# Kernel tuning notes

Measured on AMD Instinct MI355X. Metric: run time of the kernel, lower is better.

Reference implementation:

```python
import math
import jax, jax.numpy as jnp
import numpy as np

DIM = 4096
N_HEADS = 32
N_KV_HEADS = 8
HEAD_DIM = DIM // N_HEADS  # 128
N_REP = N_HEADS // N_KV_HEADS  # 4
BSZ = 2
SEQLEN = 2048
ROPE_THETA = 500000.0


def setup_inputs() -> dict:
    key = jax.random.key(0)
    ks = jax.random.split(key, 6)
    s = 0.02
    x = jax.random.normal(ks[0], (BSZ, SEQLEN, DIM), dtype=jnp.float32)
    wq = jax.random.normal(ks[1], (DIM, N_HEADS * HEAD_DIM), dtype=jnp.float32) * s
    wk = jax.random.normal(ks[2], (DIM, N_KV_HEADS * HEAD_DIM), dtype=jnp.float32) * s
    wv = jax.random.normal(ks[3], (DIM, N_KV_HEADS * HEAD_DIM), dtype=jnp.float32) * s
    wo = jax.random.normal(ks[4], (N_HEADS * HEAD_DIM, DIM), dtype=jnp.float32) * s
    # RoPE frequencies (real cos/sin form of complex freqs_cis)
    inv_freq = 1.0 / (ROPE_THETA ** (jnp.arange(0, HEAD_DIM, 2, dtype=jnp.float32) / HEAD_DIM))
    t = jnp.arange(SEQLEN, dtype=jnp.float32)
    angles = jnp.outer(t, inv_freq)  # [S, HEAD_DIM/2]
    freqs_cos = jnp.cos(angles)
    freqs_sin = jnp.sin(angles)
    # additive causal mask [S, S]: 0 on/below diag, -1e9 above
    mask = jnp.where(jnp.tril(jnp.ones((SEQLEN, SEQLEN), dtype=bool)), 0.0, -1e9).astype(jnp.float32)
    return {"x": x, "wq": wq, "wk": wk, "wv": wv, "wo": wo,
            "freqs_cos": freqs_cos, "freqs_sin": freqs_sin, "mask": mask,
            "start_pos": 0}


def _apply_rope(t, cos, sin):
    # t: [B, S, H, HD]; cos/sin: [S, HD/2] -> broadcast [1, S, 1, HD/2]
    b, s, h, hd = t.shape
    tr = t.reshape(b, s, h, hd // 2, 2)
    te, to = tr[..., 0], tr[..., 1]
    c = cos[None, :, None, :]
    sn = sin[None, :, None, :]
    oe = te * c - to * sn
    oo = te * sn + to * c
    return jnp.stack([oe, oo], axis=-1).reshape(b, s, h, hd)


def reference(x, wq, wk, wv, wo, freqs_cos, freqs_sin, mask, start_pos):
    bsz, seqlen, _ = x.shape
    xq = (x @ wq).reshape(bsz, seqlen, N_HEADS, HEAD_DIM)
    xk = (x @ wk).reshape(bsz, seqlen, N_KV_HEADS, HEAD_DIM)
    xv = (x @ wv).reshape(bsz, seqlen, N_KV_HEADS, HEAD_DIM)
    xq = _apply_rope(xq, freqs_cos, freqs_sin)
    xk = _apply_rope(xk, freqs_cos, freqs_sin)
    # prefill: cache[:start_pos+seqlen] == xk/xv (start_pos=0); GQA repeat
    keys = jnp.repeat(xk, N_REP, axis=2)    # [B, S, N_HEADS, HD]
    values = jnp.repeat(xv, N_REP, axis=2)
    q = xq.transpose(0, 2, 1, 3)            # [B, H, S, HD]
    k = keys.transpose(0, 2, 1, 3)
    v = values.transpose(0, 2, 1, 3)
    scores = jnp.einsum('bhqd,bhkd->bhqk', q, k) / math.sqrt(HEAD_DIM)
    scores = scores + mask[None, None, :, :]
    probs = jax.nn.softmax(scores.astype(jnp.float32), axis=-1).astype(q.dtype)
    ctx = jnp.einsum('bhqk,bhkd->bhqd', probs, v)
    out = ctx.transpose(0, 2, 1, 3).reshape(bsz, seqlen, N_HEADS * HEAD_DIM)
    return out @ wo
```

## Files before the change

kernel.cpp:

```cpp
#include <hip/hip_runtime.h>
#include <hip/hip_bf16.h>
#include <math.h>
#include <stdint.h>

#define DIM 4096
#define N_HEADS 32
#define N_KV_HEADS 8
#define HEAD_DIM 128
#define BSZ 2
#define SEQLEN 2048
#define BS (BSZ * SEQLEN)
#define KV_DIM (N_KV_HEADS * HEAD_DIM)

typedef unsigned short u16;
typedef __attribute__((ext_vector_type(8))) short bf16x8;
typedef __attribute__((ext_vector_type(4))) float f32x4;
typedef __attribute__((ext_vector_type(8))) unsigned short u16x8;
typedef __attribute__((ext_vector_type(4))) unsigned short u16x4;

__device__ __forceinline__ u16 f2bf(float f) {
    __hip_bfloat16 h = __float2bfloat16(f);
    return *reinterpret_cast<u16*>(&h);
}
__device__ __forceinline__ float bf2f(u16 u) {
    __hip_bfloat16 h;
    *reinterpret_cast<u16*>(&h) = u;
    return __bfloat162float(h);
}

#define GLOAD_LDS16(gptr, lptr)                                                      \
    __builtin_amdgcn_global_load_lds(                                                \
        reinterpret_cast<const __attribute__((address_space(1))) uint32_t*>(         \
            reinterpret_cast<uintptr_t>(gptr)),                                      \
        reinterpret_cast<__attribute__((address_space(3))) uint32_t*>(               \
            reinterpret_cast<uintptr_t>(lptr)),                                      \
        16, 0, 0)

__global__ void cvt_f32_bf16(const float* __restrict__ in, u16* __restrict__ out, int n4) {
    int i = blockIdx.x * blockDim.x + threadIdx.x;
    if (i >= n4) return;
    float4 v = reinterpret_cast<const float4*>(in)[i];
    u16x4 o;
    o.x = f2bf(v.x); o.y = f2bf(v.y); o.z = f2bf(v.z); o.w = f2bf(v.w);
    reinterpret_cast<u16x4*>(out)[i] = o;
}

__global__ __launch_bounds__(256) void transpose_f32_bf16(const float* __restrict__ in,
                                                          u16* __restrict__ out,
                                                          int K, int N) {
    __shared__ float tile[32][33];
    const int tx = threadIdx.x, ty = threadIdx.y;
    const int n0 = blockIdx.x * 32, k0 = blockIdx.y * 32;
#pragma unroll
    for (int i = 0; i < 4; ++i)
        tile[ty + 8 * i][tx] = in[(size_t)(k0 + ty + 8 * i) * N + n0 + tx];
    __syncthreads();
#pragma unroll
    for (int i = 0; i < 4; ++i)
        out[(size_t)(n0 + ty + 8 * i) * K + k0 + tx] = f2bf(tile[tx][ty + 8 * i]);
}

__global__ __launch_bounds__(256) void transpose_v_bf16(const u16* __restrict__ xv,
                                                        u16* __restrict__ xvT) {
    __shared__ u16 tile[32][33];
    const int tx = threadIdx.x, ty = threadIdx.y;
    const int k0 = blockIdx.x * 32, d0 = blockIdx.y * 32;
    const int bh = blockIdx.z;
    const int b = bh >> 3, hkv = bh & 7;
#pragma unroll
    for (int i = 0; i < 4; ++i)
        tile[ty + 8 * i][tx] =
            xv[((size_t)(b * SEQLEN) + k0 + ty + 8 * i) * KV_DIM + hkv * HEAD_DIM + d0 + tx];
    __syncthreads();
#pragma unroll
    for (int i = 0; i < 4; ++i)
        xvT[((size_t)bh * HEAD_DIM + d0 + ty + 8 * i) * SEQLEN + k0 + tx] = tile[tx][ty + 8 * i];
}

template <bool OUT_BF16>
__global__ __launch_bounds__(256) void gemm_mfma_bt(const u16* __restrict__ A,
                                                    const u16* __restrict__ BT,
                                                    void* __restrict__ Cv,
                                                    int M, int N, int K) {
    __shared__ __align__(16) u16 Al[128 * 64];
    __shared__ __align__(16) u16 Bl[128 * 64];

    const int tid  = threadIdx.x;
    const int wave = tid >> 6;
    const int lane = tid & 63;
    const int quad = lane >> 4;
    const int lm   = lane & 15;
    const size_t bm = (size_t)blockIdx.y * 128;
    const size_t bn = (size_t)blockIdx.x * 128;
    const int wm = (wave & 1) * 64;
    const int wn = (wave >> 1) * 64;

    const int slot = lane & 7;
    const int lrow = lane >> 3;
    const int csw  = slot ^ (lrow & 7);

    f32x4 acc[4][4] = {};

    for (int k0 = 0; k0 < K; k0 += 64) {
        __syncthreads();
#pragma unroll
        for (int i = 0; i < 4; ++i) {
            const int mloc = wave * 32 + i * 8 + lrow;
            const u16* gA = A  + (bm + mloc) * (size_t)K + k0 + csw * 8;
            const u16* gB = BT + (bn + mloc) * (size_t)K + k0 + csw * 8;
            u16* lA = &Al[(mloc * 8 + slot) * 8];
            u16* lB = &Bl[(mloc * 8 + slot) * 8];
            GLOAD_LDS16(gA, lA);
            GLOAD_LDS16(gB, lB);
        }
        __syncthreads();

#pragma unroll
        for (int ks8 = 0; ks8 < 8; ks8 += 4) {
            bf16x8 af[4], bfr[4];
            const int cc = ks8 + quad;
#pragma unroll
            for (int i = 0; i < 4; ++i) {
                const int m = wm + 16 * i + lm;
                af[i]  = *(const bf16x8*)&Al[(m * 8 + (cc ^ (m & 7))) * 8];
                const int n = wn + 16 * i + lm;
                bfr[i] = *(const bf16x8*)&Bl[(n * 8 + (cc ^ (n & 7))) * 8];
            }
#pragma unroll
            for (int i = 0; i < 4; ++i)
#pragma unroll
                for (int j = 0; j < 4; ++j)
                    acc[i][j] = __builtin_amdgcn_mfma_f32_16x16x32_bf16(af[i], bfr[j], acc[i][j], 0, 0, 0);
        }
    }

#pragma unroll
    for (int i = 0; i < 4; ++i) {
        const int mrow = wm + 16 * i + quad * 4;
#pragma unroll
        for (int j = 0; j < 4; ++j) {
            const int ncol = wn + 16 * j + lm;
#pragma unroll
            for (int r = 0; r < 4; ++r) {
                const size_t off = (bm + mrow + r) * (size_t)N + bn + ncol;
                const float v = acc[i][j][r];
                if constexpr (OUT_BF16) ((u16*)Cv)[off] = f2bf(v);
                else                    ((float*)Cv)[off] = v;
            }
        }
    }
}

__global__ void rope_kernel(u16* __restrict__ t,
                            const float* __restrict__ cosb,
                            const float* __restrict__ sinb,
                            int n_heads, int total_pairs) {
    int idx = blockIdx.x * blockDim.x + threadIdx.x;
    if (idx >= total_pairs) return;
    int p = idx & 63;
    int h = (idx >> 6) % n_heads;
    int bs = idx / (64 * n_heads);
    int s = bs & (SEQLEN - 1);

    float c = cosb[s * 64 + p];
    float sn = sinb[s * 64 + p];

    size_t base = (size_t)bs * (n_heads * HEAD_DIM) + h * HEAD_DIM + 2 * p;
    float e = bf2f(t[base]);
    float o = bf2f(t[base + 1]);
    t[base]     = f2bf(e * c - o * sn);
    t[base + 1] = f2bf(e * sn + o * c);
}

__global__ __launch_bounds__(256) void flash_attn_mfma(const u16* __restrict__ xq,
                                                       const u16* __restrict__ xk,
                                                       const u16* __restrict__ xvT,
                                                       u16* __restrict__ ctx) {
    __shared__ __align__(16) u16 Ks[64 * 16 * 8];
    __shared__ __align__(16) u16 Vt[128 * 8 * 8];
    __shared__ __align__(16) u16 Ps[4][16 * 8 * 8];

    const int qt  = blockIdx.x;
    const int h   = blockIdx.y;
    const int b   = blockIdx.z;
    const int hkv = h >> 2;

    const int tid  = threadIdx.x;
    const int wave = tid >> 6;
    const int lane = tid & 63;
    const int quad = lane >> 4;
    const int lm   = lane & 15;
    const int q0   = qt * 64;
    const float scale = 0.08838834764831845f;

    bf16x8 qf[4];
    {
        const u16* qp = xq + ((size_t)(b * SEQLEN) + q0 + wave * 16 + lm) * DIM
                        + h * HEAD_DIM + quad * 8;
#pragma unroll
        for (int s = 0; s < 4; ++s) qf[s] = *(const bf16x8*)(qp + s * 32);
    }

    float m_i[4], l_i[4];
#pragma unroll
    for (int r = 0; r < 4; ++r) { m_i[r] = -INFINITY; l_i[r] = 0.f; }
    f32x4 acc_o[8] = {};

    for (int kt = 0; kt <= qt; ++kt) {
        const int k0 = kt * 64;
        __syncthreads();
#pragma unroll
        for (int i = 0; i < 4; ++i) {
            const int ci = i * 256 + tid;
            const int kr = ci >> 4, cp = ci & 15;
            const u16* gK = xk + ((size_t)(b * SEQLEN + k0 + kr)) * KV_DIM
                            + hkv * HEAD_DIM + (cp ^ (kr & 7)) * 8;
            GLOAD_LDS16(gK, &Ks[ci * 8]);
            const int dr = ci >> 3, cq = ci & 7;
            const u16* gV = xvT + (((size_t)(b * N_KV_HEADS + hkv)) * HEAD_DIM + dr) * SEQLEN
                            + k0 + (cq ^ (dr & 7)) * 8;
            GLOAD_LDS16(gV, &Vt[ci * 8]);
        }
        __syncthreads();

        f32x4 sacc[4] = {};
#pragma unroll
        for (int ks = 0; ks < 4; ++ks) {
#pragma unroll
            for (int ct = 0; ct < 4; ++ct) {
                const int krow = ct * 16 + lm;
                bf16x8 kf = *(const bf16x8*)&Ks[(krow * 16 + ((ks * 4 + quad) ^ (krow & 7))) * 8];
                sacc[ct] = __builtin_amdgcn_mfma_f32_16x16x32_bf16(qf[ks], kf, sacc[ct], 0, 0, 0);
            }
        }

#pragma unroll
        for (int ct = 0; ct < 4; ++ct) sacc[ct] *= scale;

        if (kt == qt) {
#pragma unroll
            for (int ct = 0; ct < 4; ++ct)
#pragma unroll
                for (int r = 0; r < 4; ++r)
                    if (k0 + ct * 16 + lm > q0 + wave * 16 + quad * 4 + r)
                        sacc[ct][r] = -1e30f;
        }

        float alpha[4];
#pragma unroll
        for (int r = 0; r < 4; ++r) {
            float mx = fmaxf(fmaxf(sacc[0][r], sacc[1][r]), fmaxf(sacc[2][r], sacc[3][r]));
#pragma unroll
            for (int off = 1; off < 16; off <<= 1) mx = fmaxf(mx, __shfl_xor(mx, off));
            const float nm = fmaxf(m_i[r], mx);
            alpha[r] = __expf(m_i[r] - nm);
            m_i[r] = nm;
            float sum = 0.f;
#pragma unroll
            for (int ct = 0; ct < 4; ++ct) {
                const float p = __expf(sacc[ct][r] - nm);
                sacc[ct][r] = p;
                sum += p;
            }
#pragma unroll
            for (int off = 1; off < 16; off <<= 1) sum += __shfl_xor(sum, off);
            l_i[r] = alpha[r] * l_i[r] + sum;
        }

        u16* ps = &Ps[wave][0];
#pragma unroll
        for (int ct = 0; ct < 4; ++ct)
#pragma unroll
            for (int r = 0; r < 4; ++r) {
                const int q   = quad * 4 + r;
                const int col = ct * 16 + lm;
                ps[(q * 8 + ((col >> 3) ^ (q & 7))) * 8 + (col & 7)] = f2bf(sacc[ct][r]);
            }
        bf16x8 pf[2];
#pragma unroll
        for (int ks = 0; ks < 2; ++ks)
            pf[ks] = *(const bf16x8*)&ps[(lm * 8 + ((ks * 4 + quad) ^ (lm & 7))) * 8];

#pragma unroll
        for (int dt = 0; dt < 8; ++dt)
#pragma unroll
            for (int r = 0; r < 4; ++r) acc_o[dt][r] *= alpha[r];

#pragma unroll
        for (int ks = 0; ks < 2; ++ks)
#pragma unroll
            for (int dt = 0; dt < 8; ++dt) {
                const int d = dt * 16 + lm;
                bf16x8 vf = *(const bf16x8*)&Vt[(d * 8 + ((ks * 4 + quad) ^ (d & 7))) * 8];
                acc_o[dt] = __builtin_amdgcn_mfma_f32_16x16x32_bf16(pf[ks], vf, acc_o[dt], 0, 0, 0);
            }
    }

    float inv_l[4];
#pragma unroll
    for (int r = 0; r < 4; ++r) inv_l[r] = 1.f / l_i[r];
    u16* op = ctx + ((size_t)(b * SEQLEN) + q0 + wave * 16 + quad * 4) * DIM + h * HEAD_DIM + lm;
#pragma unroll
    for (int r = 0; r < 4; ++r)
#pragma unroll
        for (int dt = 0; dt < 8; ++dt)
            op[(size_t)r * DIM + dt * 16] = f2bf(acc_o[dt][r] * inv_l[r]);
}

extern "C" void kernel_launch(void* const* d_in, const int* in_sizes, int n_in,
                              void* d_out, int out_size, void* d_ws, size_t ws_size,
                              hipStream_t stream) {
    const float* x   = (const float*)d_in[0];
    const float* wq  = (const float*)d_in[1];
    const float* wk  = (const float*)d_in[2];
    const float* wv  = (const float*)d_in[3];
    const float* wo  = (const float*)d_in[4];
    const float* fc  = (const float*)d_in[5];
    const float* fs  = (const float*)d_in[6];
    float* out = (float*)d_out;

    u16* x_bf = (u16*)d_ws;
    u16* wqT  = x_bf + (size_t)BS * DIM;
    u16* wkT  = wqT + (size_t)DIM * DIM;
    u16* wvT  = wkT + (size_t)KV_DIM * DIM;
    u16* woT  = wvT + (size_t)KV_DIM * DIM;
    u16* xq   = woT + (size_t)DIM * DIM;
    u16* xk   = xq + (size_t)BS * DIM;
    u16* xv   = xk + (size_t)BS * KV_DIM;
    u16* ctx  = x_bf;
    u16* xvT  = wvT;

    {
        int n4 = BS * DIM / 4;
        cvt_f32_bf16<<<(n4 + 255) / 256, 256, 0, stream>>>(x, x_bf, n4);
        dim3 blk(32, 8);
        transpose_f32_bf16<<<dim3(DIM / 32, DIM / 32), blk, 0, stream>>>(wq, wqT, DIM, DIM);
        transpose_f32_bf16<<<dim3(KV_DIM / 32, DIM / 32), blk, 0, stream>>>(wk, wkT, DIM, KV_DIM);
        transpose_f32_bf16<<<dim3(KV_DIM / 32, DIM / 32), blk, 0, stream>>>(wv, wvT, DIM, KV_DIM);
        transpose_f32_bf16<<<dim3(DIM / 32, DIM / 32), blk, 0, stream>>>(wo, woT, DIM, DIM);
    }

    gemm_mfma_bt<true><<<dim3(DIM / 128, BS / 128), 256, 0, stream>>>(x_bf, wqT, xq, BS, DIM, DIM);
    gemm_mfma_bt<true><<<dim3(KV_DIM / 128, BS / 128), 256, 0, stream>>>(x_bf, wkT, xk, BS, KV_DIM, DIM);
    gemm_mfma_bt<true><<<dim3(KV_DIM / 128, BS / 128), 256, 0, stream>>>(x_bf, wvT, xv, BS, KV_DIM, DIM);

    transpose_v_bf16<<<dim3(SEQLEN / 32, HEAD_DIM / 32, BSZ * N_KV_HEADS), dim3(32, 8), 0, stream>>>(xv, xvT);

    {
        int total_q = BS * N_HEADS * 64;
        rope_kernel<<<(total_q + 255) / 256, 256, 0, stream>>>(xq, fc, fs, N_HEADS, total_q);
        int total_k = BS * N_KV_HEADS * 64;
        rope_kernel<<<(total_k + 255) / 256, 256, 0, stream>>>(xk, fc, fs, N_KV_HEADS, total_k);
    }

    flash_attn_mfma<<<dim3(SEQLEN / 64, N_HEADS, BSZ), 256, 0, stream>>>(xq, xk, xvT, ctx);

    gemm_mfma_bt<false><<<dim3(DIM / 128, BS / 128), 256, 0, stream>>>(ctx, woT, out, BS, DIM, DIM);
}
```

Measured before the change: 1.112 ms.

## Enlarge attention query tile to 128 rows, reverse block order, use exp2

The flash attention kernel now gives each block 128 query rows, with each wave handling two 16-row groups. Every K/V tile loaded into LDS is therefore reused across twice as many queries, which halves the K/V global loads and the per-tile barrier overhead. Blocks are launched in reverse so the longest causal rows start first, softmax uses exp2 with the scale folded into one constant, and s_setprio raises wave priority around the MFMA loops. The cost is higher register and LDS use per block, fewer total blocks, and some waves idling on the last diagonal tiles via the early continue.

```diff
diff --git a/kernel.cpp b/kernel.cpp
--- a/kernel.cpp
+++ b/kernel.cpp
@@ -178,9 +178,9 @@
                                                        u16* __restrict__ ctx) {
     __shared__ __align__(16) u16 Ks[64 * 16 * 8];
     __shared__ __align__(16) u16 Vt[128 * 8 * 8];
-    __shared__ __align__(16) u16 Ps[4][16 * 8 * 8];
-
-    const int qt  = blockIdx.x;
+    __shared__ __align__(16) u16 Ps[4][32 * 8 * 8];
+
+    const int qt  = (int)gridDim.x - 1 - (int)blockIdx.x;
     const int h   = blockIdx.y;
     const int b   = blockIdx.z;
     const int hkv = h >> 2;
@@ -190,23 +190,28 @@
     const int lane = tid & 63;
     const int quad = lane >> 4;
     const int lm   = lane & 15;
-    const int q0   = qt * 64;
-    const float scale = 0.08838834764831845f;
-
-    bf16x8 qf[4];
-    {
-        const u16* qp = xq + ((size_t)(b * SEQLEN) + q0 + wave * 16 + lm) * DIM
+    const int q0   = qt * 128;
+    const int wq0  = q0 + wave * 32;
+    const float C = 0.08838834764831845f * 1.44269504088896f;
+
+    bf16x8 qf[2][4];
+#pragma unroll
+    for (int g = 0; g < 2; ++g) {
+        const u16* qp = xq + ((size_t)(b * SEQLEN) + wq0 + g * 16 + lm) * DIM
                         + h * HEAD_DIM + quad * 8;
 #pragma unroll
-        for (int s = 0; s < 4; ++s) qf[s] = *(const bf16x8*)(qp + s * 32);
-    }
-
-    float m_i[4], l_i[4];
-#pragma unroll
-    for (int r = 0; r < 4; ++r) { m_i[r] = -INFINITY; l_i[r] = 0.f; }
-    f32x4 acc_o[8] = {};
-
-    for (int kt = 0; kt <= qt; ++kt) {
+        for (int s = 0; s < 4; ++s) qf[g][s] = *(const bf16x8*)(qp + s * 32);
+    }
+
+    float m_i[2][4], l_i[2][4];
+#pragma unroll
+    for (int g = 0; g < 2; ++g)
+#pragma unroll
+        for (int r = 0; r < 4; ++r) { m_i[g][r] = -INFINITY; l_i[g][r] = 0.f; }
+    f32x4 acc_o[2][8] = {};
+
+    const int nkt = 2 * qt + 2;
+    for (int kt = 0; kt < nkt; ++kt) {
         const int k0 = kt * 64;
         __syncthreads();
 #pragma unroll
@@ -223,88 +228,110 @@
         }
         __syncthreads();
 
-        f32x4 sacc[4] = {};
+        if (k0 > wq0 + 31) continue;
+
+        f32x4 sacc[2][4] = {};
+        __builtin_amdgcn_s_setprio(1);
 #pragma unroll
         for (int ks = 0; ks < 4; ++ks) {
 #pragma unroll
             for (int ct = 0; ct < 4; ++ct) {
                 const int krow = ct * 16 + lm;
                 bf16x8 kf = *(const bf16x8*)&Ks[(krow * 16 + ((ks * 4 + quad) ^ (krow & 7))) * 8];
-                sacc[ct] = __builtin_amdgcn_mfma_f32_16x16x32_bf16(qf[ks], kf, sacc[ct], 0, 0, 0);
-            }
-        }
-
-#pragma unroll
-        for (int ct = 0; ct < 4; ++ct) sacc[ct] *= scale;
-
-        if (kt == qt) {
+                sacc[0][ct] = __builtin_amdgcn_mfma_f32_16x16x32_bf16(qf[0][ks], kf, sacc[0][ct], 0, 0, 0);
+                sacc[1][ct] = __builtin_amdgcn_mfma_f32_16x16x32_bf16(qf[1][ks], kf, sacc[1][ct], 0, 0, 0);
+            }
+        }
+        __builtin_amdgcn_s_setprio(0);
+
+#pragma unroll
+        for (int g = 0; g < 2; ++g) {
+            if (k0 + 63 > wq0 + g * 16) {
+#pragma unroll
+                for (int ct = 0; ct < 4; ++ct)
+#pragma unroll
+                    for (int r = 0; r < 4; ++r)
+                        if (k0 + ct * 16 + lm > wq0 + g * 16 + quad * 4 + r)
+                            sacc[g][ct][r] = -1e30f;
+            }
+        }
+
+        float alpha[2][4];
+#pragma unroll
+        for (int g = 0; g < 2; ++g)
+#pragma unroll
+            for (int r = 0; r < 4; ++r) {
+                float mx = fmaxf(fmaxf(sacc[g][0][r], sacc[g][1][r]),
+                                 fmaxf(sacc[g][2][r], sacc[g][3][r]));
+#pragma unroll
+                for (int off = 1; off < 16; off <<= 1) mx = fmaxf(mx, __shfl_xor(mx, off));
+                const float nm = fmaxf(m_i[g][r], mx);
+                alpha[g][r] = exp2f((m_i[g][r] - nm) * C);
+                m_i[g][r] = nm;
+                float sum = 0.f;
+#pragma unroll
+                for (int ct = 0; ct < 4; ++ct) {
+                    const float p = exp2f((sacc[g][ct][r] - nm) * C);
+                    sacc[g][ct][r] = p;
+                    sum += p;
+                }
+#pragma unroll
+                for (int off = 1; off < 16; off <<= 1) sum += __shfl_xor(sum, off);
+                l_i[g][r] = alpha[g][r] * l_i[g][r] + sum;
+            }
+
+        u16* ps = &Ps[wave][0];
+#pragma unroll
+        for (int g = 0; g < 2; ++g)
 #pragma unroll
             for (int ct = 0; ct < 4; ++ct)
 #pragma unroll
-                for (int r = 0; r < 4; ++r)
-                    if (k0 + ct * 16 + lm > q0 + wave * 16 + quad * 4 + r)
-                        sacc[ct][r] = -1e30f;
-        }
-
-        float alpha[4];
-#pragma unroll
-        for (int r = 0; r < 4; ++r) {
-            float mx = fmaxf(fmaxf(sacc[0][r], sacc[1][r]), fmaxf(sacc[2][r], sacc[3][r]));
-#pragma unroll
-            for (int off = 1; off < 16; off <<= 1) mx = fmaxf(mx, __shfl_xor(mx, off));
-            const float nm = fmaxf(m_i[r], mx);
-            alpha[r] = __expf(m_i[r] - nm);
-            m_i[r] = nm;
-            float sum = 0.f;
-#pragma unroll
-            for (int ct = 0; ct < 4; ++ct) {
-                const float p = __expf(sacc[ct][r] - nm);
-                sacc[ct][r] = p;
-                sum += p;
-            }
-#pragma unroll
-            for (int off = 1; off < 16; off <<= 1) sum += __shfl_xor(sum, off);
-            l_i[r] = alpha[r] * l_i[r] + sum;
-        }
-
-        u16* ps = &Ps[wave][0];
-#pragma unroll
-        for (int ct = 0; ct < 4; ++ct)
-#pragma unroll
-            for (int r = 0; r < 4; ++r) {
-                const int q   = quad * 4 + r;
-                const int col = ct * 16 + lm;
-                ps[(q * 8 + ((col >> 3) ^ (q & 7))) * 8 + (col & 7)] = f2bf(sacc[ct][r]);
-            }
-        bf16x8 pf[2];
-#pragma unroll
-        for (int ks = 0; ks < 2; ++ks)
-            pf[ks] = *(const bf16x8*)&ps[(lm * 8 + ((ks * 4 + quad) ^ (lm & 7))) * 8];
-
-#pragma unroll
-        for (int dt = 0; dt < 8; ++dt)
-#pragma unroll
-            for (int r = 0; r < 4; ++r) acc_o[dt][r] *= alpha[r];
-
+                for (int r = 0; r < 4; ++r) {
+                    const int qq  = g * 16 + quad * 4 + r;
+                    const int col = ct * 16 + lm;
+                    ps[(qq * 8 + ((col >> 3) ^ (qq & 7))) * 8 + (col & 7)] = f2bf(sacc[g][ct][r]);
+                }
+        bf16x8 pf[2][2];
+#pragma unroll
+        for (int g = 0; g < 2; ++g) {
+            const int qq = g * 16 + lm;
+#pragma unroll
+            for (int ks = 0; ks < 2; ++ks)
+                pf[g][ks] = *(const bf16x8*)&ps[(qq * 8 + ((ks * 4 + quad) ^ (qq & 7))) * 8];
+        }
+
+#pragma unroll
+        for (int g = 0; g < 2; ++g)
+#pragma unroll
+            for (int dt = 0; dt < 8; ++dt)
+#pragma unroll
+                for (int r = 0; r < 4; ++r) acc_o[g][dt][r] *= alpha[g][r];
+
+        __builtin_amdgcn_s_setprio(1);
 #pragma unroll
         for (int ks = 0; ks < 2; ++ks)
 #pragma unroll
             for (int dt = 0; dt < 8; ++dt) {
                 const int d = dt * 16 + lm;
                 bf16x8 vf = *(const bf16x8*)&Vt[(d * 8 + ((ks * 4 + quad) ^ (d & 7))) * 8];
-                acc_o[dt] = __builtin_amdgcn_mfma_f32_16x16x32_bf16(pf[ks], vf, acc_o[dt], 0, 0, 0);
-            }
-    }
-
-    float inv_l[4];
-#pragma unroll
-    for (int r = 0; r < 4; ++r) inv_l[r] = 1.f / l_i[r];
-    u16* op = ctx + ((size_t)(b * SEQLEN) + q0 + wave * 16 + quad * 4) * DIM + h * HEAD_DIM + lm;
-#pragma unroll
-    for (int r = 0; r < 4; ++r)
-#pragma unroll
-        for (int dt = 0; dt < 8; ++dt)
-            op[(size_t)r * DIM + dt * 16] = f2bf(acc_o[dt][r] * inv_l[r]);
+                acc_o[0][dt] = __builtin_amdgcn_mfma_f32_16x16x32_bf16(pf[0][ks], vf, acc_o[0][dt], 0, 0, 0);
+                acc_o[1][dt] = __builtin_amdgcn_mfma_f32_16x16x32_bf16(pf[1][ks], vf, acc_o[1][dt], 0, 0, 0);
+            }
+        __builtin_amdgcn_s_setprio(0);
+    }
+
+#pragma unroll
+    for (int g = 0; g < 2; ++g) {
+        float inv_l[4];
+#pragma unroll
+        for (int r = 0; r < 4; ++r) inv_l[r] = 1.f / l_i[g][r];
+        u16* op = ctx + ((size_t)(b * SEQLEN) + wq0 + g * 16 + quad * 4) * DIM + h * HEAD_DIM + lm;
+#pragma unroll
+        for (int r = 0; r < 4; ++r)
+#pragma unroll
+            for (int dt = 0; dt < 8; ++dt)
+                op[(size_t)r * DIM + dt * 16] = f2bf(acc_o[g][dt][r] * inv_l[r]);
+    }
 }
 
 extern "C" void kernel_launch(void* const* d_in, const int* in_sizes, int n_in,
@@ -353,7 +380,7 @@
         rope_kernel<<<(total_k + 255) / 256, 256, 0, stream>>>(xk, fc, fs, N_KV_HEADS, total_k);
     }
 
-    flash_attn_mfma<<<dim3(SEQLEN / 64, N_HEADS, BSZ), 256, 0, stream>>>(xq, xk, xvT, ctx);
+    flash_attn_mfma<<<dim3(SEQLEN / 128, N_HEADS, BSZ), 256, 0, stream>>>(xq, xk, xvT, ctx);
 
     gemm_mfma_bt<false><<<dim3(DIM / 128, BS / 128), 256, 0, stream>>>(ctx, woT, out, BS, DIM, DIM);
 }
```

Result: slower. 1.281 ms (+15.2%).

## Double-buffer K/V tiles in flash attention and schedule longest query tiles first

Applied to the files above, without the earlier changes.

The attention kernel now keeps two LDS buffers for K and V, so the global-to-LDS load of the next key tile is issued before computing on the current one, leaving one barrier per iteration instead of two. Query tiles are visited in reverse block order so the longest causal rows start first, which should even out the load tail. The softmax scale is folded into exp2 with a log2e constant, and MFMA regions are wrapped in s_setprio. This doubles the K/V LDS footprint, which may lower occupancy.

```diff
diff --git a/kernel.cpp b/kernel.cpp
--- a/kernel.cpp
+++ b/kernel.cpp
@@ -176,11 +176,11 @@
                                                        const u16* __restrict__ xk,
                                                        const u16* __restrict__ xvT,
                                                        u16* __restrict__ ctx) {
-    __shared__ __align__(16) u16 Ks[64 * 16 * 8];
-    __shared__ __align__(16) u16 Vt[128 * 8 * 8];
+    __shared__ __align__(16) u16 Ks[2][64 * 16 * 8];
+    __shared__ __align__(16) u16 Vt[2][128 * 8 * 8];
     __shared__ __align__(16) u16 Ps[4][16 * 8 * 8];
 
-    const int qt  = blockIdx.x;
+    const int qt  = (int)gridDim.x - 1 - (int)blockIdx.x;
     const int h   = blockIdx.y;
     const int b   = blockIdx.z;
     const int hkv = h >> 2;
@@ -191,7 +191,10 @@
     const int quad = lane >> 4;
     const int lm   = lane & 15;
     const int q0   = qt * 64;
-    const float scale = 0.08838834764831845f;
+    const float C = 0.08838834764831845f * 1.44269504088896f;
+
+    const int ciK_r[4] = { (0 * 256 + tid) >> 4, (1 * 256 + tid) >> 4,
+                           (2 * 256 + tid) >> 4, (3 * 256 + tid) >> 4 };
 
     bf16x8 qf[4];
     {
@@ -201,41 +204,50 @@
         for (int s = 0; s < 4; ++s) qf[s] = *(const bf16x8*)(qp + s * 32);
     }
 
-    float m_i[4], l_i[4];
-#pragma unroll
-    for (int r = 0; r < 4; ++r) { m_i[r] = -INFINITY; l_i[r] = 0.f; }
-    f32x4 acc_o[8] = {};
-
-    for (int kt = 0; kt <= qt; ++kt) {
+    const u16* xkb = xk + (size_t)(b * SEQLEN) * KV_DIM + hkv * HEAD_DIM;
+    const u16* xvb = xvT + ((size_t)(b * N_KV_HEADS + hkv)) * HEAD_DIM * SEQLEN;
+
+    auto STAGE = [&](int kt, int sel) {
         const int k0 = kt * 64;
-        __syncthreads();
 #pragma unroll
         for (int i = 0; i < 4; ++i) {
             const int ci = i * 256 + tid;
             const int kr = ci >> 4, cp = ci & 15;
-            const u16* gK = xk + ((size_t)(b * SEQLEN + k0 + kr)) * KV_DIM
-                            + hkv * HEAD_DIM + (cp ^ (kr & 7)) * 8;
-            GLOAD_LDS16(gK, &Ks[ci * 8]);
+            const u16* gK = xkb + (size_t)(k0 + kr) * KV_DIM + (cp ^ (kr & 7)) * 8;
+            GLOAD_LDS16(gK, &Ks[sel][ci * 8]);
             const int dr = ci >> 3, cq = ci & 7;
-            const u16* gV = xvT + (((size_t)(b * N_KV_HEADS + hkv)) * HEAD_DIM + dr) * SEQLEN
-                            + k0 + (cq ^ (dr & 7)) * 8;
-            GLOAD_LDS16(gV, &Vt[ci * 8]);
-        }
-        __syncthreads();
-
+            const u16* gV = xvb + (size_t)dr * SEQLEN + k0 + (cq ^ (dr & 7)) * 8;
+            GLOAD_LDS16(gV, &Vt[sel][ci * 8]);
+        }
+    };
+
+    float m_i[4], l_i[4];
+#pragma unroll
+    for (int r = 0; r < 4; ++r) { m_i[r] = -INFINITY; l_i[r] = 0.f; }
+    f32x4 acc_o[8] = {};
+
+    STAGE(0, 0);
+    __syncthreads();
+
+    for (int kt = 0; kt <= qt; ++kt) {
+        const int sel = kt & 1;
+        const int k0 = kt * 64;
+        if (kt < qt) STAGE(kt + 1, sel ^ 1);
+
+        const u16* ksb = &Ks[sel][0];
+        const u16* vtb = &Vt[sel][0];
         f32x4 sacc[4] = {};
+        __builtin_amdgcn_s_setprio(1);
 #pragma unroll
         for (int ks = 0; ks < 4; ++ks) {
 #pragma unroll
             for (int ct = 0; ct < 4; ++ct) {
                 const int krow = ct * 16 + lm;
-                bf16x8 kf = *(const bf16x8*)&Ks[(krow * 16 + ((ks * 4 + quad) ^ (krow & 7))) * 8];
+                bf16x8 kf = *(const bf16x8*)&ksb[(krow * 16 + ((ks * 4 + quad) ^ (krow & 7))) * 8];
                 sacc[ct] = __builtin_amdgcn_mfma_f32_16x16x32_bf16(qf[ks], kf, sacc[ct], 0, 0, 0);
             }
         }
-
-#pragma unroll
-        for (int ct = 0; ct < 4; ++ct) sacc[ct] *= scale;
+        __builtin_amdgcn_s_setprio(0);
 
         if (kt == qt) {
 #pragma unroll
@@ -253,12 +265,12 @@
 #pragma unroll
             for (int off = 1; off < 16; off <<= 1) mx = fmaxf(mx, __shfl_xor(mx, off));
             const float nm = fmaxf(m_i[r], mx);
-            alpha[r] = __expf(m_i[r] - nm);
+            alpha[r] = exp2f((m_i[r] - nm) * C);
             m_i[r] = nm;
             float sum = 0.f;
 #pragma unroll
             for (int ct = 0; ct < 4; ++ct) {
-                const float p = __expf(sacc[ct][r] - nm);
+                const float p = exp2f((sacc[ct][r] - nm) * C);
                 sacc[ct][r] = p;
                 sum += p;
             }
@@ -272,9 +284,9 @@
         for (int ct = 0; ct < 4; ++ct)
 #pragma unroll
             for (int r = 0; r < 4; ++r) {
-                const int q   = quad * 4 + r;
+                const int qq  = quad * 4 + r;
                 const int col = ct * 16 + lm;
-                ps[(q * 8 + ((col >> 3) ^ (q & 7))) * 8 + (col & 7)] = f2bf(sacc[ct][r]);
+                ps[(qq * 8 + ((col >> 3) ^ (qq & 7))) * 8 + (col & 7)] = f2bf(sacc[ct][r]);
             }
         bf16x8 pf[2];
 #pragma unroll
@@ -286,14 +298,18 @@
 #pragma unroll
             for (int r = 0; r < 4; ++r) acc_o[dt][r] *= alpha[r];
 
+        __builtin_amdgcn_s_setprio(1);
 #pragma unroll
         for (int ks = 0; ks < 2; ++ks)
 #pragma unroll
             for (int dt = 0; dt < 8; ++dt) {
                 const int d = dt * 16 + lm;
-                bf16x8 vf = *(const bf16x8*)&Vt[(d * 8 + ((ks * 4 + quad) ^ (d & 7))) * 8];
+                bf16x8 vf = *(const bf16x8*)&vtb[(d * 8 + ((ks * 4 + quad) ^ (d & 7))) * 8];
                 acc_o[dt] = __builtin_amdgcn_mfma_f32_16x16x32_bf16(pf[ks], vf, acc_o[dt], 0, 0, 0);
             }
+        __builtin_amdgcn_s_setprio(0);
+
+        if (kt < qt) __syncthreads();
     }
 
     float inv_l[4];
```

New measurement: 1.133 ms. No clear change (+1.9%).
